# Kernel tuning notes

Hardware: AMD Instinct MI355X
Metric: run time of the kernel (lower is better)

The kernel has to match this reference:

```python
import jax, jax.numpy as jnp
import numpy as np

N, E, IN_CH, EDGE_DIM, OUT_CH = 50000, 600000, 128, 64, 128


def setup_inputs() -> dict:
    key = jax.random.key(0)
    ks = jax.random.split(key, 9)
    return {
        "x": jax.random.normal(ks[0], (N, IN_CH), dtype=jnp.float32),
        "edge_index": jax.random.randint(ks[1], (2, E), 0, N, dtype=jnp.int64),
        "edge_attr": jax.random.normal(ks[2], (E, EDGE_DIM), dtype=jnp.float32),
        "Wx": jax.random.normal(ks[3], (IN_CH, OUT_CH), dtype=jnp.float32) * 0.05,
        "bx": jax.random.normal(ks[4], (OUT_CH,), dtype=jnp.float32) * 0.05,
        "We": jax.random.normal(ks[5], (EDGE_DIM, OUT_CH), dtype=jnp.float32) * 0.05,
        "be": jax.random.normal(ks[6], (OUT_CH,), dtype=jnp.float32) * 0.05,
        "Wm": jax.random.normal(ks[7], (2 * OUT_CH, OUT_CH), dtype=jnp.float32) * 0.05,
        "bm": jax.random.normal(ks[8], (OUT_CH,), dtype=jnp.float32) * 0.05,
        "beta": jnp.float32(0.1),
    }


def reference(x, edge_index, edge_attr, Wx, bx, We, be, Wm, bm, beta):
    # node / edge projections
    xp = x @ Wx + bx                      # [N, out]
    ef = edge_attr @ We + be              # [E, out]
    src, dst = edge_index[0], edge_index[1]
    # gather source node features, combine with edge features
    msg = jnp.concatenate([xp[src], ef], axis=1)   # [E, 2*out]
    msg = jax.nn.leaky_relu(msg @ Wm + bm)         # slope 0.01 matches torch default
    # scatter-add into destination nodes
    agg = jax.ops.segment_sum(msg, dst, num_segments=xp.shape[0])  # [N, out]
    return jax.nn.sigmoid(agg) * jax.nn.relu(beta)
```

## Files before the change

kernel.cpp:

```cpp
#include <hip/hip_runtime.h>


#define NB 25000
#define NB_SHIFT 1
#define TPW 4

typedef __bf16 bf16x8 __attribute__((ext_vector_type(8)));
typedef float  f32x4  __attribute__((ext_vector_type(4)));
typedef unsigned short ushort_t;
typedef unsigned int   uint_t;

__device__ __forceinline__ ushort_t f2b(float f) {
    uint_t u = __float_as_uint(f);
    u += 0x7FFF + ((u >> 16) & 1);
    return (ushort_t)(u >> 16);
}
__device__ __forceinline__ uint_t pack2(float a, float b) {
    return (uint_t)f2b(a) | ((uint_t)f2b(b) << 16);
}

__global__ void fuse_weights_kernel(const float* __restrict__ Wx,
                                    const float* __restrict__ bx,
                                    const float* __restrict__ We,
                                    const float* __restrict__ be,
                                    const float* __restrict__ Wm,
                                    const float* __restrict__ bm,
                                    ushort_t* __restrict__ WxmT16,
                                    ushort_t* __restrict__ WemT16,
                                    float* __restrict__ bf) {
    int idx = blockIdx.x * blockDim.x + threadIdx.x;
    if (idx < 128 * 128) {
        int r = idx >> 7, c = idx & 127;
        float acc = 0.f;
        #pragma unroll 8
        for (int j = 0; j < 128; ++j) acc += Wx[r * 128 + j] * Wm[j * 128 + c];
        WxmT16[c * 128 + r] = f2b(acc);
    } else if (idx < 128 * 128 + 64 * 128) {
        int t = idx - 128 * 128;
        int r = t >> 7, c = t & 127;
        float acc = 0.f;
        #pragma unroll 8
        for (int j = 0; j < 128; ++j) acc += We[r * 128 + j] * Wm[(128 + j) * 128 + c];
        WemT16[c * 64 + r] = f2b(acc);
    } else if (idx < 128 * 128 + 64 * 128 + 128) {
        int c = idx - (128 * 128 + 64 * 128);
        float acc = bm[c];
        #pragma unroll 8
        for (int j = 0; j < 128; ++j)
            acc += bx[j] * Wm[j * 128 + c] + be[j] * Wm[(128 + j) * 128 + c];
        bf[c] = acc;
    }
}

__global__ __launch_bounds__(256) void node_gemm_kernel(
        const float* __restrict__ x, const ushort_t* __restrict__ WxmT16,
        const float* __restrict__ bf, ushort_t* __restrict__ ub, int N) {
    int tid = threadIdx.x;
    int g = blockIdx.x * 4 + (tid >> 6);
    if (g >= (N / 16) * 2) return;
    int lane = tid & 63, l15 = lane & 15, quad = lane >> 4;
    int n0 = (g >> 1) * 16;
    int chBase = (g & 1) * 64;

    bf16x8 B[4][4];
    #pragma unroll
    for (int ct = 0; ct < 4; ++ct)
        #pragma unroll
        for (int kk = 0; kk < 4; ++kk)
            B[ct][kk] = __builtin_bit_cast(bf16x8, *((const uint4*)
                &WxmT16[(size_t)(chBase + ct * 16 + l15) * 128 + kk * 32 + quad * 8]));

    bf16x8 A[4];
    #pragma unroll
    for (int kk = 0; kk < 4; ++kk) {
        const float4* s = (const float4*)&x[(size_t)(n0 + l15) * 128 + kk * 32 + quad * 8];
        float4 v0 = s[0], v1 = s[1];
        uint4 w;
        w.x = pack2(v0.x, v0.y);
        w.y = pack2(v0.z, v0.w);
        w.z = pack2(v1.x, v1.y);
        w.w = pack2(v1.z, v1.w);
        A[kk] = __builtin_bit_cast(bf16x8, w);
    }

    f32x4 acc[4] = {{0.f,0.f,0.f,0.f},{0.f,0.f,0.f,0.f},
                    {0.f,0.f,0.f,0.f},{0.f,0.f,0.f,0.f}};
    #pragma unroll
    for (int kk = 0; kk < 4; ++kk)
        #pragma unroll
        for (int ct = 0; ct < 4; ++ct)
            acc[ct] = __builtin_amdgcn_mfma_f32_16x16x32_bf16(A[kk], B[ct][kk], acc[ct], 0, 0, 0);

    #pragma unroll
    for (int ct = 0; ct < 4; ++ct) {
        float bias = bf[chBase + ct * 16 + l15];
        #pragma unroll
        for (int r = 0; r < 4; ++r)
            ub[(size_t)(n0 + quad * 4 + r) * 128 + chBase + ct * 16 + l15] =
                f2b(acc[ct][r] + bias);
    }
}

__global__ __launch_bounds__(1024) void hist_kernel(
        const int* __restrict__ ei, int* __restrict__ cnt, int E) {
    __shared__ int lcnt[NB];
    int t = threadIdx.x;
    for (int i = t; i < NB; i += 1024) lcnt[i] = 0;
    __syncthreads();
    int base = blockIdx.x * 8192;
    #pragma unroll
    for (int j = 0; j < 8; ++j) {
        int e = base + t + j * 1024;
        if (e < E) atomicAdd(&lcnt[ei[E + e] >> NB_SHIFT], 1);
    }
    __syncthreads();
    for (int i = t; i < NB; i += 1024) {
        int c = lcnt[i];
        if (c) atomicAdd(&cnt[i], c);
    }
}

__global__ __launch_bounds__(1024) void scan_kernel(
        const int* __restrict__ cnt, int* __restrict__ start,
        int* __restrict__ cur, int nb, int E) {
    __shared__ int tot[1024];
    int t = threadIdx.x;
    int v[25]; int sum = 0;
    #pragma unroll
    for (int j = 0; j < 25; ++j) {
        int i = t * 25 + j;
        v[j] = (i < nb) ? cnt[i] : 0;
        sum += v[j];
    }
    tot[t] = sum;
    __syncthreads();
    for (int d = 1; d < 1024; d <<= 1) {
        int val = tot[t];
        int add = (t >= d) ? tot[t - d] : 0;
        __syncthreads();
        tot[t] = val + add;
        __syncthreads();
    }
    int ex = (t == 0) ? 0 : tot[t - 1];
    #pragma unroll
    for (int j = 0; j < 25; ++j) {
        int i = t * 25 + j;
        if (i < nb) { start[i] = ex; cur[i] = ex; }
        ex += v[j];
    }
    if (t == 1023) start[nb] = ex;
}

__global__ __launch_bounds__(1024) void binpos_kernel(
        const int* __restrict__ ei, int* __restrict__ cur,
        int* __restrict__ pos, uint_t* __restrict__ recs, int E) {
    __shared__ int lcnt[NB];
    int t = threadIdx.x;
    for (int i = t; i < NB; i += 1024) lcnt[i] = 0;
    __syncthreads();
    int base = blockIdx.x * 8192;
    int myrank[8], mybkt[8];
    #pragma unroll
    for (int j = 0; j < 8; ++j) {
        int e = base + t + j * 1024;
        if (e < E) {
            int b = ei[E + e] >> NB_SHIFT;
            mybkt[j] = b;
            myrank[j] = atomicAdd(&lcnt[b], 1);
        }
    }
    __syncthreads();
    for (int i = t; i < NB; i += 1024) {
        int c = lcnt[i];
        lcnt[i] = c ? atomicAdd(&cur[i], c) : 0;
    }
    __syncthreads();
    #pragma unroll
    for (int j = 0; j < 8; ++j) {
        int e = base + t + j * 1024;
        if (e < E) {
            int p = lcnt[mybkt[j]] + myrank[j];
            pos[e] = p;
            uint_t src  = (uint_t)ei[e];
            uint_t dstl = (uint_t)(ei[E + e] & ((1 << NB_SHIFT) - 1));
            recs[p] = src | (dstl << 16);
        }
    }
}

__global__ __launch_bounds__(256) void msg_stream_kernel(
        const float* __restrict__ ea, const int* __restrict__ pos,
        const ushort_t* __restrict__ WemT16, ushort_t* __restrict__ msgl, int E) {
    int tid = threadIdx.x;
    int g = blockIdx.x * 4 + (tid >> 6);
    int grp = g >> 1;
    int chBase = (g & 1) << 6;
    int t0 = grp * (TPW * 16);
    if (t0 >= E) return;
    int lane = tid & 63, l15 = lane & 15, quad = lane >> 4;

    bf16x8 B[4][2];
    #pragma unroll
    for (int ct = 0; ct < 4; ++ct)
        #pragma unroll
        for (int kk = 0; kk < 2; ++kk)
            B[ct][kk] = __builtin_bit_cast(bf16x8, *((const uint4*)
                &WemT16[(size_t)(chBase + ct * 16 + l15) * 64 + kk * 32 + quad * 8]));

    #pragma unroll
    for (int tt = 0; tt < TPW; ++tt) {
        int t16 = t0 + tt * 16;
        if (t16 >= E) break;
        const float* rowp = &ea[(size_t)(t16 + l15) * 64];
        const float4* sA = (const float4*)(rowp + quad * 8);
        float4 v0 = sA[0], v1 = sA[1];
        uint4 w0;
        w0.x = pack2(v0.x, v0.y);
        w0.y = pack2(v0.z, v0.w);
        w0.z = pack2(v1.x, v1.y);
        w0.w = pack2(v1.z, v1.w);
        bf16x8 a0 = __builtin_bit_cast(bf16x8, w0);
        const float4* sB = (const float4*)(rowp + 32 + quad * 8);
        float4 v2 = sB[0], v3 = sB[1];
        uint4 w1;
        w1.x = pack2(v2.x, v2.y);
        w1.y = pack2(v2.z, v2.w);
        w1.z = pack2(v3.x, v3.y);
        w1.w = pack2(v3.z, v3.w);
        bf16x8 a1 = __builtin_bit_cast(bf16x8, w1);

        f32x4 acc[4] = {{0.f,0.f,0.f,0.f},{0.f,0.f,0.f,0.f},
                        {0.f,0.f,0.f,0.f},{0.f,0.f,0.f,0.f}};
        #pragma unroll
        for (int ct = 0; ct < 4; ++ct)
            acc[ct] = __builtin_amdgcn_mfma_f32_16x16x32_bf16(a0, B[ct][0], acc[ct], 0, 0, 0);
        #pragma unroll
        for (int ct = 0; ct < 4; ++ct)
            acc[ct] = __builtin_amdgcn_mfma_f32_16x16x32_bf16(a1, B[ct][1], acc[ct], 0, 0, 0);

        int4 pr = *(const int4*)&pos[t16 + quad * 4];
        int prr[4] = {pr.x, pr.y, pr.z, pr.w};
        #pragma unroll
        for (int r = 0; r < 4; ++r) {
            #pragma unroll
            for (int ct = 0; ct < 4; ++ct)
                msgl[(size_t)prr[r] * 128 + chBase + ct * 16 + l15] = f2b(acc[ct][r]);
        }
    }
}

__global__ __launch_bounds__(256) void segsum_kernel(
        const ushort_t* __restrict__ msgl, const ushort_t* __restrict__ ub,
        const uint_t* __restrict__ recs, const int* __restrict__ start,
        const float* __restrict__ beta, float* __restrict__ out, int N) {
    int wid = blockIdx.x * 4 + (threadIdx.x >> 6);
    if (wid >= NB) return;
    int lane = threadIdx.x & 63;
    int half = lane >> 5;
    int c8 = lane & 31;

    int s0 = start[wid], s1 = start[wid + 1];
    float a0[4] = {0.f, 0.f, 0.f, 0.f};
    float a1[4] = {0.f, 0.f, 0.f, 0.f};

    int p = s0 + half;
    uint_t rec = (p < s1) ? recs[p] : 0u;
    while (p < s1) {
        int pn = p + 2;
        uint_t recn = (pn < s1) ? recs[pn] : 0u;

        uint2 mv = *(const uint2*)&msgl[(size_t)p * 128 + (c8 << 2)];
        int sr = (int)(rec & 0xFFFFu);
        uint2 uv = *(const uint2*)&ub[(size_t)sr * 128 + (c8 << 2)];

        float w1 = (rec >> 16) ? 1.f : 0.f;
        float w0 = 1.f - w1;

        float m0 = __uint_as_float(mv.x << 16)         + __uint_as_float(uv.x << 16);
        float m1 = __uint_as_float(mv.x & 0xFFFF0000u) + __uint_as_float(uv.x & 0xFFFF0000u);
        float m2 = __uint_as_float(mv.y << 16)         + __uint_as_float(uv.y << 16);
        float m3 = __uint_as_float(mv.y & 0xFFFF0000u) + __uint_as_float(uv.y & 0xFFFF0000u);
        m0 = fmaxf(m0, 0.01f * m0);
        m1 = fmaxf(m1, 0.01f * m1);
        m2 = fmaxf(m2, 0.01f * m2);
        m3 = fmaxf(m3, 0.01f * m3);

        a0[0] += m0 * w0;  a1[0] += m0 * w1;
        a0[1] += m1 * w0;  a1[1] += m1 * w1;
        a0[2] += m2 * w0;  a1[2] += m2 * w1;
        a0[3] += m3 * w0;  a1[3] += m3 * w1;

        p = pn; rec = recn;
    }

    #pragma unroll
    for (int j = 0; j < 4; ++j) {
        a0[j] += __shfl_xor(a0[j], 32);
        a1[j] += __shfl_xor(a1[j], 32);
    }

    float rb = beta[0];
    rb = rb > 0.f ? rb : 0.f;
    int n = (wid << 1) + half;
    if (n < N) {
        float4 v;
        if (half == 0) {
            v.x = a0[0]; v.y = a0[1]; v.z = a0[2]; v.w = a0[3];
        } else {
            v.x = a1[0]; v.y = a1[1]; v.z = a1[2]; v.w = a1[3];
        }
        v.x = rb / (1.f + __expf(-v.x));
        v.y = rb / (1.f + __expf(-v.y));
        v.z = rb / (1.f + __expf(-v.z));
        v.w = rb / (1.f + __expf(-v.w));
        ((float4*)out)[(size_t)n * 32 + c8] = v;
    }
}

extern "C" void kernel_launch(void* const* d_in, const int* in_sizes, int n_in,
                              void* d_out, int out_size, void* d_ws, size_t ws_size,
                              hipStream_t stream) {
    const float* x    = (const float*)d_in[0];
    const int*   ei   = (const int*)d_in[1];
    const float* ea   = (const float*)d_in[2];
    const float* Wx   = (const float*)d_in[3];
    const float* bx   = (const float*)d_in[4];
    const float* We   = (const float*)d_in[5];
    const float* be   = (const float*)d_in[6];
    const float* Wm   = (const float*)d_in[7];
    const float* bm   = (const float*)d_in[8];
    const float* beta = (const float*)d_in[9];

    int N = in_sizes[0] / 128;
    int E = in_sizes[2] / 64;

    float* out = (float*)d_out;

    char* ws = (char*)d_ws;
    ushort_t* WxmT16 = (ushort_t*)(ws);
    ushort_t* WemT16 = (ushort_t*)(ws + 32768);
    float*    bf     = (float*)(ws + 49152);
    ushort_t* ub     = (ushort_t*)(ws + 65536);
    size_t off = 65536 + (size_t)N * 128 * 2;
    uint_t* recs   = (uint_t*)(ws + off);
    off += (size_t)E * 4;
    int* pos       = (int*)(ws + off);
    off += (size_t)E * 4;
    int* cnt       = (int*)(ws + off);
    int* startb    = (int*)(ws + off + 131072);
    int* cur       = (int*)(ws + off + 262144);
    ushort_t* msgl = (ushort_t*)(ws + off + 393216);

    hipMemsetAsync(cnt, 0, (size_t)NB * sizeof(int), stream);

    fuse_weights_kernel<<<(24704 + 255) / 256, 256, 0, stream>>>(
        Wx, bx, We, be, Wm, bm, WxmT16, WemT16, bf);

    node_gemm_kernel<<<(N / 16 * 2 + 3) / 4, 256, 0, stream>>>(
        x, WxmT16, bf, ub, N);

    int nbBlocks = (E + 8191) / 8192;
    hist_kernel<<<nbBlocks, 1024, 0, stream>>>(ei, cnt, E);
    scan_kernel<<<1, 1024, 0, stream>>>(cnt, startb, cur, NB, E);
    binpos_kernel<<<nbBlocks, 1024, 0, stream>>>(ei, cur, pos, recs, E);

    int ntile  = (E + 15) / 16;
    int ngrp   = (ntile + TPW - 1) / TPW;
    int nwaves = ngrp * 2;
    msg_stream_kernel<<<(nwaves + 3) / 4, 256, 0, stream>>>(
        ea, pos, WemT16, msgl, E);

    segsum_kernel<<<(NB + 3) / 4, 256, 0, stream>>>(
        msgl, ub, recs, startb, beta, out, N);
}
```

Baseline: 481.0 us.

## Transpose MFMA outputs for vector stores and widen segsum gathers with prefetch

```diff
diff --git a/kernel.cpp b/kernel.cpp
--- a/kernel.cpp
+++ b/kernel.cpp
@@ -89,15 +89,16 @@
     for (int kk = 0; kk < 4; ++kk)
         #pragma unroll
         for (int ct = 0; ct < 4; ++ct)
-            acc[ct] = __builtin_amdgcn_mfma_f32_16x16x32_bf16(A[kk], B[ct][kk], acc[ct], 0, 0, 0);
+            acc[ct] = __builtin_amdgcn_mfma_f32_16x16x32_bf16(B[ct][kk], A[kk], acc[ct], 0, 0, 0);
 
     #pragma unroll
     for (int ct = 0; ct < 4; ++ct) {
-        float bias = bf[chBase + ct * 16 + l15];
-        #pragma unroll
-        for (int r = 0; r < 4; ++r)
-            ub[(size_t)(n0 + quad * 4 + r) * 128 + chBase + ct * 16 + l15] =
-                f2b(acc[ct][r] + bias);
+        int ch = chBase + ct * 16 + quad * 4;
+        float4 bv = *(const float4*)&bf[ch];
+        uint2 w;
+        w.x = pack2(acc[ct][0] + bv.x, acc[ct][1] + bv.y);
+        w.y = pack2(acc[ct][2] + bv.z, acc[ct][3] + bv.w);
+        *((uint2*)&ub[(size_t)(n0 + l15) * 128 + ch]) = w;
     }
 }
 
@@ -107,9 +108,9 @@
     int t = threadIdx.x;
     for (int i = t; i < NB; i += 1024) lcnt[i] = 0;
     __syncthreads();
-    int base = blockIdx.x * 8192;
-    #pragma unroll
-    for (int j = 0; j < 8; ++j) {
+    int base = blockIdx.x * 16384;
+    #pragma unroll
+    for (int j = 0; j < 16; ++j) {
         int e = base + t + j * 1024;
         if (e < E) atomicAdd(&lcnt[ei[E + e] >> NB_SHIFT], 1);
     }
@@ -158,10 +159,10 @@
     int t = threadIdx.x;
     for (int i = t; i < NB; i += 1024) lcnt[i] = 0;
     __syncthreads();
-    int base = blockIdx.x * 8192;
-    int myrank[8], mybkt[8];
-    #pragma unroll
-    for (int j = 0; j < 8; ++j) {
+    int base = blockIdx.x * 16384;
+    int myrank[16], mybkt[16];
+    #pragma unroll
+    for (int j = 0; j < 16; ++j) {
         int e = base + t + j * 1024;
         if (e < E) {
             int b = ei[E + e] >> NB_SHIFT;
@@ -176,7 +177,7 @@
     }
     __syncthreads();
     #pragma unroll
-    for (int j = 0; j < 8; ++j) {
+    for (int j = 0; j < 16; ++j) {
         int e = base + t + j * 1024;
         if (e < E) {
             int p = lcnt[mybkt[j]] + myrank[j];
@@ -207,44 +208,87 @@
             B[ct][kk] = __builtin_bit_cast(bf16x8, *((const uint4*)
                 &WemT16[(size_t)(chBase + ct * 16 + l15) * 64 + kk * 32 + quad * 8]));
 
-    #pragma unroll
-    for (int tt = 0; tt < TPW; ++tt) {
-        int t16 = t0 + tt * 16;
-        if (t16 >= E) break;
-        const float* rowp = &ea[(size_t)(t16 + l15) * 64];
-        const float4* sA = (const float4*)(rowp + quad * 8);
-        float4 v0 = sA[0], v1 = sA[1];
-        uint4 w0;
-        w0.x = pack2(v0.x, v0.y);
-        w0.y = pack2(v0.z, v0.w);
-        w0.z = pack2(v1.x, v1.y);
-        w0.w = pack2(v1.z, v1.w);
-        bf16x8 a0 = __builtin_bit_cast(bf16x8, w0);
-        const float4* sB = (const float4*)(rowp + 32 + quad * 8);
-        float4 v2 = sB[0], v3 = sB[1];
-        uint4 w1;
-        w1.x = pack2(v2.x, v2.y);
-        w1.y = pack2(v2.z, v2.w);
-        w1.z = pack2(v3.x, v3.y);
-        w1.w = pack2(v3.z, v3.w);
-        bf16x8 a1 = __builtin_bit_cast(bf16x8, w1);
-
-        f32x4 acc[4] = {{0.f,0.f,0.f,0.f},{0.f,0.f,0.f,0.f},
-                        {0.f,0.f,0.f,0.f},{0.f,0.f,0.f,0.f}};
+    if (t0 + TPW * 16 <= E) {
+        bf16x8 a0[TPW], a1[TPW];
+        int pr[TPW];
         #pragma unroll
-        for (int ct = 0; ct < 4; ++ct)
-            acc[ct] = __builtin_amdgcn_mfma_f32_16x16x32_bf16(a0, B[ct][0], acc[ct], 0, 0, 0);
+        for (int tt = 0; tt < TPW; ++tt) {
+            int t16 = t0 + tt * 16;
+            const float* rowp = &ea[(size_t)(t16 + l15) * 64];
+            const float4* sA = (const float4*)(rowp + quad * 8);
+            float4 v0 = sA[0], v1 = sA[1];
+            uint4 w0;
+            w0.x = pack2(v0.x, v0.y);
+            w0.y = pack2(v0.z, v0.w);
+            w0.z = pack2(v1.x, v1.y);
+            w0.w = pack2(v1.z, v1.w);
+            a0[tt] = __builtin_bit_cast(bf16x8, w0);
+            const float4* sB = (const float4*)(rowp + 32 + quad * 8);
+            float4 v2 = sB[0], v3 = sB[1];
+            uint4 w1;
+            w1.x = pack2(v2.x, v2.y);
+            w1.y = pack2(v2.z, v2.w);
+            w1.z = pack2(v3.x, v3.y);
+            w1.w = pack2(v3.z, v3.w);
+            a1[tt] = __builtin_bit_cast(bf16x8, w1);
+            pr[tt] = pos[t16 + l15];
+        }
         #pragma unroll
-        for (int ct = 0; ct < 4; ++ct)
-            acc[ct] = __builtin_amdgcn_mfma_f32_16x16x32_bf16(a1, B[ct][1], acc[ct], 0, 0, 0);
-
-        int4 pr = *(const int4*)&pos[t16 + quad * 4];
-        int prr[4] = {pr.x, pr.y, pr.z, pr.w};
-        #pragma unroll
-        for (int r = 0; r < 4; ++r) {
+        for (int tt = 0; tt < TPW; ++tt) {
+            f32x4 acc[4] = {{0.f,0.f,0.f,0.f},{0.f,0.f,0.f,0.f},
+                            {0.f,0.f,0.f,0.f},{0.f,0.f,0.f,0.f}};
             #pragma unroll
             for (int ct = 0; ct < 4; ++ct)
-                msgl[(size_t)prr[r] * 128 + chBase + ct * 16 + l15] = f2b(acc[ct][r]);
+                acc[ct] = __builtin_amdgcn_mfma_f32_16x16x32_bf16(B[ct][0], a0[tt], acc[ct], 0, 0, 0);
+            #pragma unroll
+            for (int ct = 0; ct < 4; ++ct)
+                acc[ct] = __builtin_amdgcn_mfma_f32_16x16x32_bf16(B[ct][1], a1[tt], acc[ct], 0, 0, 0);
+            #pragma unroll
+            for (int ct = 0; ct < 4; ++ct) {
+                uint2 w;
+                w.x = pack2(acc[ct][0], acc[ct][1]);
+                w.y = pack2(acc[ct][2], acc[ct][3]);
+                *((uint2*)&msgl[(size_t)pr[tt] * 128 + chBase + ct * 16 + quad * 4]) = w;
+            }
+        }
+    } else {
+        for (int tt = 0; tt < TPW; ++tt) {
+            int t16 = t0 + tt * 16;
+            if (t16 >= E) break;
+            const float* rowp = &ea[(size_t)(t16 + l15) * 64];
+            const float4* sA = (const float4*)(rowp + quad * 8);
+            float4 v0 = sA[0], v1 = sA[1];
+            uint4 w0;
+            w0.x = pack2(v0.x, v0.y);
+            w0.y = pack2(v0.z, v0.w);
+            w0.z = pack2(v1.x, v1.y);
+            w0.w = pack2(v1.z, v1.w);
+            bf16x8 a0 = __builtin_bit_cast(bf16x8, w0);
+            const float4* sB = (const float4*)(rowp + 32 + quad * 8);
+            float4 v2 = sB[0], v3 = sB[1];
+            uint4 w1;
+            w1.x = pack2(v2.x, v2.y);
+            w1.y = pack2(v2.z, v2.w);
+            w1.z = pack2(v3.x, v3.y);
+            w1.w = pack2(v3.z, v3.w);
+            bf16x8 a1 = __builtin_bit_cast(bf16x8, w1);
+            int pr = pos[t16 + l15];
+
+            f32x4 acc[4] = {{0.f,0.f,0.f,0.f},{0.f,0.f,0.f,0.f},
+                            {0.f,0.f,0.f,0.f},{0.f,0.f,0.f,0.f}};
+            #pragma unroll
+            for (int ct = 0; ct < 4; ++ct)
+                acc[ct] = __builtin_amdgcn_mfma_f32_16x16x32_bf16(B[ct][0], a0, acc[ct], 0, 0, 0);
+            #pragma unroll
+            for (int ct = 0; ct < 4; ++ct)
+                acc[ct] = __builtin_amdgcn_mfma_f32_16x16x32_bf16(B[ct][1], a1, acc[ct], 0, 0, 0);
+            #pragma unroll
+            for (int ct = 0; ct < 4; ++ct) {
+                uint2 w;
+                w.x = pack2(acc[ct][0], acc[ct][1]);
+                w.y = pack2(acc[ct][2], acc[ct][3]);
+                *((uint2*)&msgl[(size_t)pr * 128 + chBase + ct * 16 + quad * 4]) = w;
+            }
         }
     }
 }
@@ -256,64 +300,88 @@
     int wid = blockIdx.x * 4 + (threadIdx.x >> 6);
     if (wid >= NB) return;
     int lane = threadIdx.x & 63;
-    int half = lane >> 5;
-    int c8 = lane & 31;
+    int q = lane >> 4;
+    int c16 = lane & 15;
 
     int s0 = start[wid], s1 = start[wid + 1];
-    float a0[4] = {0.f, 0.f, 0.f, 0.f};
-    float a1[4] = {0.f, 0.f, 0.f, 0.f};
-
-    int p = s0 + half;
-    uint_t rec = (p < s1) ? recs[p] : 0u;
-    while (p < s1) {
-        int pn = p + 2;
-        uint_t recn = (pn < s1) ? recs[pn] : 0u;
-
-        uint2 mv = *(const uint2*)&msgl[(size_t)p * 128 + (c8 << 2)];
-        int sr = (int)(rec & 0xFFFFu);
-        uint2 uv = *(const uint2*)&ub[(size_t)sr * 128 + (c8 << 2)];
-
-        float w1 = (rec >> 16) ? 1.f : 0.f;
+    float a0[8] = {0.f,0.f,0.f,0.f,0.f,0.f,0.f,0.f};
+    float a1[8] = {0.f,0.f,0.f,0.f,0.f,0.f,0.f,0.f};
+
+    int pA = s0 + q;
+    uint_t recA = (pA < s1) ? recs[pA] : 0u;
+    int pB = pA + 4;
+    uint_t recB = (pB < s1) ? recs[pB] : 0u;
+
+    int pcA = (pA < s1) ? pA : 0;
+    uint4 mvA = *(const uint4*)&msgl[(size_t)pcA * 128 + (c16 << 3)];
+    uint4 uvA = *(const uint4*)&ub[(size_t)(recA & 0xFFFFu) * 128 + (c16 << 3)];
+
+    while (pA < s1) {
+        int pC = pB + 4;
+        uint_t recC = (pC < s1) ? recs[pC] : 0u;
+        int pcB = (pB < s1) ? pB : pcA;
+        uint4 mvB = *(const uint4*)&msgl[(size_t)pcB * 128 + (c16 << 3)];
+        uint4 uvB = *(const uint4*)&ub[(size_t)(recB & 0xFFFFu) * 128 + (c16 << 3)];
+
+        float w1 = (recA >> 16) ? 1.f : 0.f;
         float w0 = 1.f - w1;
-
-        float m0 = __uint_as_float(mv.x << 16)         + __uint_as_float(uv.x << 16);
-        float m1 = __uint_as_float(mv.x & 0xFFFF0000u) + __uint_as_float(uv.x & 0xFFFF0000u);
-        float m2 = __uint_as_float(mv.y << 16)         + __uint_as_float(uv.y << 16);
-        float m3 = __uint_as_float(mv.y & 0xFFFF0000u) + __uint_as_float(uv.y & 0xFFFF0000u);
-        m0 = fmaxf(m0, 0.01f * m0);
-        m1 = fmaxf(m1, 0.01f * m1);
-        m2 = fmaxf(m2, 0.01f * m2);
-        m3 = fmaxf(m3, 0.01f * m3);
-
-        a0[0] += m0 * w0;  a1[0] += m0 * w1;
-        a0[1] += m1 * w0;  a1[1] += m1 * w1;
-        a0[2] += m2 * w0;  a1[2] += m2 * w1;
-        a0[3] += m3 * w0;  a1[3] += m3 * w1;
-
-        p = pn; rec = recn;
-    }
-
-    #pragma unroll
-    for (int j = 0; j < 4; ++j) {
+        {
+            float mlo, mhi;
+            mlo = __uint_as_float(mvA.x << 16)         + __uint_as_float(uvA.x << 16);
+            mhi = __uint_as_float(mvA.x & 0xFFFF0000u) + __uint_as_float(uvA.x & 0xFFFF0000u);
+            mlo = fmaxf(mlo, 0.01f * mlo); mhi = fmaxf(mhi, 0.01f * mhi);
+            a0[0] += mlo * w0; a1[0] += mlo * w1;
+            a0[1] += mhi * w0; a1[1] += mhi * w1;
+            mlo = __uint_as_float(mvA.y << 16)         + __uint_as_float(uvA.y << 16);
+            mhi = __uint_as_float(mvA.y & 0xFFFF0000u) + __uint_as_float(uvA.y & 0xFFFF0000u);
+            mlo = fmaxf(mlo, 0.01f * mlo); mhi = fmaxf(mhi, 0.01f * mhi);
+            a0[2] += mlo * w0; a1[2] += mlo * w1;
+            a0[3] += mhi * w0; a1[3] += mhi * w1;
+            mlo = __uint_as_float(mvA.z << 16)         + __uint_as_float(uvA.z << 16);
+            mhi = __uint_as_float(mvA.z & 0xFFFF0000u) + __uint_as_float(uvA.z & 0xFFFF0000u);
+            mlo = fmaxf(mlo, 0.01f * mlo); mhi = fmaxf(mhi, 0.01f * mhi);
+            a0[4] += mlo * w0; a1[4] += mlo * w1;
+            a0[5] += mhi * w0; a1[5] += mhi * w1;
+            mlo = __uint_as_float(mvA.w << 16)         + __uint_as_float(uvA.w << 16);
+            mhi = __uint_as_float(mvA.w & 0xFFFF0000u) + __uint_as_float(uvA.w & 0xFFFF0000u);
+            mlo = fmaxf(mlo, 0.01f * mlo); mhi = fmaxf(mhi, 0.01f * mhi);
+            a0[6] += mlo * w0; a1[6] += mlo * w1;
+            a0[7] += mhi * w0; a1[7] += mhi * w1;
+        }
+
+        pcA = pcB;
+        pA = pB; recA = recB; mvA = mvB; uvA = uvB;
+        pB = pC; recB = recC;
+    }
+
+    #pragma unroll
+    for (int j = 0; j < 8; ++j) {
+        a0[j] += __shfl_xor(a0[j], 16);
         a0[j] += __shfl_xor(a0[j], 32);
+        a1[j] += __shfl_xor(a1[j], 16);
         a1[j] += __shfl_xor(a1[j], 32);
     }
 
     float rb = beta[0];
     rb = rb > 0.f ? rb : 0.f;
-    int n = (wid << 1) + half;
+    int h   = lane >> 5;
+    int sub = (lane >> 4) & 1;
+    int n = (wid << 1) + h;
     if (n < N) {
+        float x0, x1, x2, x3;
+        if (h == 0) {
+            if (sub == 0) { x0 = a0[0]; x1 = a0[1]; x2 = a0[2]; x3 = a0[3]; }
+            else          { x0 = a0[4]; x1 = a0[5]; x2 = a0[6]; x3 = a0[7]; }
+        } else {
+            if (sub == 0) { x0 = a1[0]; x1 = a1[1]; x2 = a1[2]; x3 = a1[3]; }
+            else          { x0 = a1[4]; x1 = a1[5]; x2 = a1[6]; x3 = a1[7]; }
+        }
         float4 v;
-        if (half == 0) {
-            v.x = a0[0]; v.y = a0[1]; v.z = a0[2]; v.w = a0[3];
-        } else {
-            v.x = a1[0]; v.y = a1[1]; v.z = a1[2]; v.w = a1[3];
-        }
-        v.x = rb / (1.f + __expf(-v.x));
-        v.y = rb / (1.f + __expf(-v.y));
-        v.z = rb / (1.f + __expf(-v.z));
-        v.w = rb / (1.f + __expf(-v.w));
-        ((float4*)out)[(size_t)n * 32 + c8] = v;
+        v.x = rb / (1.f + __expf(-x0));
+        v.y = rb / (1.f + __expf(-x1));
+        v.z = rb / (1.f + __expf(-x2));
+        v.w = rb / (1.f + __expf(-x3));
+        ((float4*)out)[(size_t)n * 32 + c16 * 2 + sub] = v;
     }
 }
 
@@ -359,7 +427,7 @@
     node_gemm_kernel<<<(N / 16 * 2 + 3) / 4, 256, 0, stream>>>(
         x, WxmT16, bf, ub, N);
 
-    int nbBlocks = (E + 8191) / 8192;
+    int nbBlocks = (E + 16383) / 16384;
     hist_kernel<<<nbBlocks, 1024, 0, stream>>>(ei, cnt, E);
     scan_kernel<<<1, 1024, 0, stream>>>(cnt, startb, cur, NB, E);
     binpos_kernel<<<nbBlocks, 1024, 0, stream>>>(ei, cur, pos, recs, E);
```

Result: faster. 467.7 us (-2.8%).
